# Performance work log

Measured on AMD Instinct MI355X. Metric: run time of the kernel, lower is better.

The kernel has to match this reference:

```python
import jax, jax.numpy as jnp
import numpy as np

ALPHA = 5.0
GAMMA = 0.5
N_BINS = 313  # standard ab-gamut bin count


def setup_inputs() -> dict:
    key = jax.random.key(0)
    k1, k2, k3, k4 = jax.random.split(key, 4)
    b, c, h, w = 4, 2, 256, 256
    inp = jax.random.normal(k1, (b, c, h, w), dtype=jnp.float32)
    # target ab values roughly in [-1, 1] (normalized ab space)
    target = 0.5 * jax.random.normal(k2, (b, c, h, w), dtype=jnp.float32)
    target = jnp.clip(target, -1.0, 1.0)
    # ab gamut bin centers in raw ab units, then normalized as in the module
    ab_raw = jax.random.uniform(k3, (N_BINS, 2), minval=-110.0, maxval=110.0, dtype=jnp.float32)
    ab_gamut = (ab_raw + 128.0) / 128.0 - 1.0
    # prior probabilities -> implied prior (rebalancing from the module __init__)
    q = jax.random.uniform(k4, (N_BINS,), minval=0.1, maxval=1.0, dtype=jnp.float32)
    prior_probs = q / jnp.sum(q)
    uni_probs = jnp.ones((N_BINS,), dtype=jnp.float32) / N_BINS
    prior_mix = (1.0 - GAMMA) * prior_probs + GAMMA * uni_probs
    prior_factor = prior_mix ** (-ALPHA)
    prior_factor = prior_factor / jnp.sum(prior_probs * prior_factor)
    implied_prior = prior_probs * prior_factor
    implied_prior = implied_prior / jnp.sum(implied_prior)
    return {"input": inp, "target": target, "ab_gamut": ab_gamut,
            "implied_prior": implied_prior.astype(jnp.float32)}


def _prior_weights(target, ab_gamut, implied_prior):
    b, c, h, w = target.shape
    tgt = target.reshape(b, c, h * w).transpose(0, 2, 1)  # [b, hw, 2]
    # squared Euclidean distances [b, Q, hw]; argmin identical to cdist argmin
    g2 = jnp.sum(ab_gamut * ab_gamut, axis=-1)            # [Q]
    t2 = jnp.sum(tgt * tgt, axis=-1)                      # [b, hw]
    cross = jnp.einsum('qd,bnd->bqn', ab_gamut, tgt)      # [b, Q, hw]
    d2 = g2[None, :, None] + t2[:, None, :] - 2.0 * cross
    nns = jnp.argmin(d2, axis=1)                          # [b, hw]
    weights = implied_prior[nns].reshape(b, 1, h, w)      # broadcast over c
    return weights


def reference(input, target, ab_gamut, implied_prior):
    l2 = (input.astype(jnp.float32) - target.astype(jnp.float32)) ** 2
    l2 = l2.astype(input.dtype)
    weights = _prior_weights(target, ab_gamut, implied_prior)  # [b,1,h,w]
    l2 = l2 * weights
    loss = jnp.mean(jnp.sum(l2, axis=(1, 2, 3)))
    return loss
```

## Files before the change

### kernel.cpp

```cpp
#include <hip/hip_runtime.h>
#include <float.h>

#define NBINS 313
#define HW    65536
#define NB    4
#define NPIX  (NB * HW)
#define HALF  (NPIX / 2)

__global__ __launch_bounds__(256) void loss_main(
    const float* __restrict__ input, const float* __restrict__ target,
    const float* __restrict__ ab, const float* __restrict__ prior,
    float* __restrict__ partials)
{
    __shared__ float4 s_bins[NBINS];
    const int tid = threadIdx.x;

    for (int i = tid; i < NBINS; i += 256) {
        float gx = ab[2 * i];
        float gy = ab[2 * i + 1];
        s_bins[i] = make_float4(gx, gy, 0.5f * (gx * gx + gy * gy), prior[i]);
    }
    __syncthreads();

    const int p0 = blockIdx.x * 256 + tid;
    const int p1 = p0 + HALF;

    const int i00 = p0 + (p0 & ~(HW - 1));
    const int i01 = i00 + HW;
    const int i10 = p1 + (p1 & ~(HW - 1));
    const int i11 = i10 + HW;

    const float tx0 = target[i00], ty0 = target[i01];
    const float tx1 = target[i10], ty1 = target[i11];
    const float ax0 = input[i00],  ay0 = input[i01];
    const float ax1 = input[i10],  ay1 = input[i11];

    const float dx0 = ax0 - tx0, dy0 = ay0 - ty0;
    const float dx1 = ax1 - tx1, dy1 = ay1 - ty1;
    const float d2_0 = dx0 * dx0 + dy0 * dy0;
    const float d2_1 = dx1 * dx1 + dy1 * dy1;

    float bf0 = FLT_MAX, bw0 = 0.0f;
    float bf1 = FLT_MAX, bw1 = 0.0f;
    for (int q = 0; q < NBINS; ++q) {
        const float4 bn = s_bins[q];
        const float f0 = fmaf(-bn.x, tx0, fmaf(-bn.y, ty0, bn.z));
        const float f1 = fmaf(-bn.x, tx1, fmaf(-bn.y, ty1, bn.z));
        const bool c0 = f0 < bf0;
        const bool c1 = f1 < bf1;
        bf0 = c0 ? f0 : bf0;  bw0 = c0 ? bn.w : bw0;
        bf1 = c1 ? f1 : bf1;  bw1 = c1 ? bn.w : bw1;
    }

    float sum = d2_0 * bw0 + d2_1 * bw1;

    for (int off = 32; off > 0; off >>= 1)
        sum += __shfl_down(sum, off);

    __shared__ float s_part[4];
    if ((tid & 63) == 0) s_part[tid >> 6] = sum;
    __syncthreads();
    if (tid == 0)
        partials[blockIdx.x] = s_part[0] + s_part[1] + s_part[2] + s_part[3];
}

__global__ __launch_bounds__(64) void loss_reduce(
    const float* __restrict__ partials, float* __restrict__ out)
{
    const int tid = threadIdx.x;
    float s = 0.0f;
    for (int i = tid; i < 512; i += 64) s += partials[i];
    for (int off = 32; off > 0; off >>= 1)
        s += __shfl_down(s, off);
    if (tid == 0) out[0] = 0.25f * s;
}

extern "C" void kernel_launch(void* const* d_in, const int* in_sizes, int n_in,
                              void* d_out, int out_size, void* d_ws, size_t ws_size,
                              hipStream_t stream)
{
    const float* input  = (const float*)d_in[0];
    const float* target = (const float*)d_in[1];
    const float* ab     = (const float*)d_in[2];
    const float* prior  = (const float*)d_in[3];
    float* out      = (float*)d_out;
    float* partials = (float*)d_ws;

    loss_main<<<HALF / 256, 256, 0, stream>>>(input, target, ab, prior, partials);
    loss_reduce<<<1, 64, 0, stream>>>(partials, out);
}
```

Before: 75.97 us.

## Pack distance and bin index into one uint for a single-min argmin

Adds a +4 bias to the per-bin score so all scores stay positive, allowing the float bits to be compared as unsigned integers. The low 9 mantissa bits are replaced with the bin index, so each iteration does one integer min instead of a compare plus two selects; the prior weight is then looked up from a separate shared array. The bin count is padded to 320 with dummy bins so the loop can be unrolled by 8. Truncating the mantissa can break near-ties differently from the exact argmin, which may pick a different bin in rare cases.

Result: no change. 76.80 us (+1.1%).

```diff
diff --git a/kernel.cpp b/kernel.cpp
--- a/kernel.cpp
+++ b/kernel.cpp
@@ -1,10 +1,10 @@
 #include <hip/hip_runtime.h>
-#include <float.h>
+#include <stdint.h>
 
 #define NBINS 313
+#define NBQ   320
 #define HW    65536
-#define NB    4
-#define NPIX  (NB * HW)
+#define NPIX  (4 * HW)
 #define HALF  (NPIX / 2)
 
 __global__ __launch_bounds__(256) void loss_main(
@@ -12,13 +12,20 @@
     const float* __restrict__ ab, const float* __restrict__ prior,
     float* __restrict__ partials)
 {
-    __shared__ float4 s_bins[NBINS];
+    __shared__ float4 s_bins[NBQ];
+    __shared__ float  s_w[NBQ];
     const int tid = threadIdx.x;
 
-    for (int i = tid; i < NBINS; i += 256) {
-        float gx = ab[2 * i];
-        float gy = ab[2 * i + 1];
-        s_bins[i] = make_float4(gx, gy, 0.5f * (gx * gx + gy * gy), prior[i]);
+    for (int i = tid; i < NBQ; i += 256) {
+        float gx = 0.0f, gy = 0.0f, z = 1e30f, w = 0.0f;
+        if (i < NBINS) {
+            gx = ab[2 * i];
+            gy = ab[2 * i + 1];
+            z  = fmaf(0.5f * gx, gx, fmaf(0.5f * gy, gy, 4.0f));
+            w  = prior[i];
+        }
+        s_bins[i] = make_float4(gx, gy, z, 0.0f);
+        s_w[i] = w;
     }
     __syncthreads();
 
@@ -40,19 +47,22 @@
     const float d2_0 = dx0 * dx0 + dy0 * dy0;
     const float d2_1 = dx1 * dx1 + dy1 * dy1;
 
-    float bf0 = FLT_MAX, bw0 = 0.0f;
-    float bf1 = FLT_MAX, bw1 = 0.0f;
-    for (int q = 0; q < NBINS; ++q) {
+    uint32_t u0 = 0xFFFFFFFFu, u1 = 0xFFFFFFFFu;
+#pragma unroll 8
+    for (int q = 0; q < NBQ; ++q) {
         const float4 bn = s_bins[q];
         const float f0 = fmaf(-bn.x, tx0, fmaf(-bn.y, ty0, bn.z));
         const float f1 = fmaf(-bn.x, tx1, fmaf(-bn.y, ty1, bn.z));
-        const bool c0 = f0 < bf0;
-        const bool c1 = f1 < bf1;
-        bf0 = c0 ? f0 : bf0;  bw0 = c0 ? bn.w : bw0;
-        bf1 = c1 ? f1 : bf1;  bw1 = c1 ? bn.w : bw1;
+        const uint32_t v0 = (__float_as_uint(f0) & ~511u) | (uint32_t)q;
+        const uint32_t v1 = (__float_as_uint(f1) & ~511u) | (uint32_t)q;
+        u0 = v0 < u0 ? v0 : u0;
+        u1 = v1 < u1 ? v1 : u1;
     }
 
-    float sum = d2_0 * bw0 + d2_1 * bw1;
+    const float bw0 = s_w[u0 & 511u];
+    const float bw1 = s_w[u1 & 511u];
+
+    float sum = fmaf(d2_0, bw0, d2_1 * bw1);
 
     for (int off = 32; off > 0; off >>= 1)
         sum += __shfl_down(sum, off);
```
